# Kernel optimization log

Measured on AMD Instinct MI355X. Metric: run time of the kernel, lower is better.

Reference implementation:

```python
import jax, jax.numpy as jnp
import numpy as np

N_NODES = 2_000_000
IN_CH = 64
OUT_CH = 128
NUM_GRAPHS = 16384


def setup_inputs() -> dict:
    key = jax.random.key(0)
    k1, k2, k3, k4 = jax.random.split(key, 4)
    x = jax.random.normal(k1, (N_NODES, IN_CH), dtype=jnp.float32)
    segment_ids = jnp.sort(
        jax.random.randint(k2, (N_NODES,), 0, NUM_GRAPHS, dtype=jnp.int64)
    )
    # nn.Linear(in, out): weight [out, in], bias [out]
    bound = 1.0 / np.sqrt(IN_CH)
    weight = jax.random.uniform(k3, (OUT_CH, IN_CH), dtype=jnp.float32,
                                minval=-bound, maxval=bound)
    bias = jax.random.uniform(k4, (OUT_CH,), dtype=jnp.float32,
                              minval=-bound, maxval=bound)
    return {"x": x, "segment_ids": segment_ids, "weight": weight,
            "bias": bias, "num_graphs": NUM_GRAPHS}


def reference(x, segment_ids, weight, bias, num_graphs):
    # Per-graph mean pooling (segment mean), then linear embed.
    sums = jax.ops.segment_sum(x, segment_ids, num_segments=num_graphs)  # [G, d]
    counts = jax.ops.segment_sum(jnp.ones((x.shape[0],), x.dtype),
                                 segment_ids, num_segments=num_graphs)  # [G]
    means = sums / counts[:, None]                                       # [G, d]
    return means @ weight.T + bias                                        # [G, out]
```

## Files before the change

kernel.cpp:

```cpp
#include <hip/hip_runtime.h>
#include <hip/hip_bf16.h>


#define IN_CH 64
#define OUT_CH 128
#define WPB 8
#define BLOCK (WPB * 64)

typedef float f32x4 __attribute__((ext_vector_type(4)));

__global__ __launch_bounds__(BLOCK) void fused_pool_linear_kernel(
        const float* __restrict__ x, const int* __restrict__ ids,
        const float* __restrict__ W, const float* __restrict__ bias,
        float* __restrict__ out, int N, int G) {
    __shared__ float w_lds[IN_CH * 129];

    const int t  = threadIdx.x;
    const int wv = t >> 6;
    const int l  = t & 63;
    const int g  = blockIdx.x * WPB + wv;

    int s0 = 0, s1 = 0;
    if (g < G) {
        const int target = g + (l & 1);
        int lo = 0, hi = N;
        const int guess = (int)(((long long)target * (long long)N) / (long long)G);
        int wlo = guess - 4096; if (wlo < 0) wlo = 0;
        int whi = guess + 4096; if (whi > N) whi = N;
        const bool ok_lo = (wlo == 0) || (ids[wlo - 1] < target);
        const bool ok_hi = (whi == N) || (ids[whi] >= target);
        if (ok_lo && ok_hi) { lo = wlo; hi = whi; }
        while (lo < hi) {
            const int mid = (lo + hi) >> 1;
            if (ids[mid] < target) lo = mid + 1; else hi = mid;
        }
        s0 = __shfl(lo, 0);
        s1 = __shfl(lo, 1);
    }

    for (int i = t; i < OUT_CH * IN_CH; i += BLOCK) {
        const int o = i >> 6;
        const int c = i & 63;
        w_lds[c * 129 + o] = W[i];
    }
    __syncthreads();

    if (g >= G) return;

    const int rs = l >> 4;
    const int cq = (l & 15) << 2;

    float4 a0 = make_float4(0.f, 0.f, 0.f, 0.f);
    float4 a1 = make_float4(0.f, 0.f, 0.f, 0.f);
    int r = s0;
    for (; r + 8 <= s1; r += 8) {
        const f32x4 v0 = __builtin_nontemporal_load(
            reinterpret_cast<const f32x4*>(x + (size_t)(r + rs) * IN_CH + cq));
        const f32x4 v1 = __builtin_nontemporal_load(
            reinterpret_cast<const f32x4*>(x + (size_t)(r + 4 + rs) * IN_CH + cq));
        a0.x += v0.x; a0.y += v0.y; a0.z += v0.z; a0.w += v0.w;
        a1.x += v1.x; a1.y += v1.y; a1.z += v1.z; a1.w += v1.w;
    }
    if (r + 4 <= s1) {
        const f32x4 v = __builtin_nontemporal_load(
            reinterpret_cast<const f32x4*>(x + (size_t)(r + rs) * IN_CH + cq));
        a0.x += v.x; a0.y += v.y; a0.z += v.z; a0.w += v.w;
        r += 4;
    }
    if (r + rs < s1) {
        const f32x4 v = __builtin_nontemporal_load(
            reinterpret_cast<const f32x4*>(x + (size_t)(r + rs) * IN_CH + cq));
        a1.x += v.x; a1.y += v.y; a1.z += v.z; a1.w += v.w;
    }

    float sx = a0.x + a1.x;
    float sy = a0.y + a1.y;
    float sz = a0.z + a1.z;
    float sw = a0.w + a1.w;

    sx += __shfl_xor(sx, 16); sy += __shfl_xor(sy, 16);
    sz += __shfl_xor(sz, 16); sw += __shfl_xor(sw, 16);
    sx += __shfl_xor(sx, 32); sy += __shfl_xor(sy, 32);
    sz += __shfl_xor(sz, 32); sw += __shfl_xor(sw, 32);

    const float cnt = (float)(s1 - s0);
    const float m0 = sx / cnt;
    const float m1 = sy / cnt;
    const float m2 = sz / cnt;
    const float m3 = sw / cnt;

    float o0 = bias[l];
    float o1 = bias[l + 64];
    #pragma unroll
    for (int c = 0; c < IN_CH; ++c) {
        float m;
        switch (c & 3) {
            case 0:  m = __shfl(m0, c >> 2); break;
            case 1:  m = __shfl(m1, c >> 2); break;
            case 2:  m = __shfl(m2, c >> 2); break;
            default: m = __shfl(m3, c >> 2); break;
        }
        o0 = fmaf(w_lds[c * 129 + l],      m, o0);
        o1 = fmaf(w_lds[c * 129 + l + 64], m, o1);
    }
    out[(size_t)g * OUT_CH + l]      = o0;
    out[(size_t)g * OUT_CH + l + 64] = o1;
}

extern "C" void kernel_launch(void* const* d_in, const int* in_sizes, int n_in,
                              void* d_out, int out_size, void* d_ws, size_t ws_size,
                              hipStream_t stream) {
    const float* x    = (const float*)d_in[0];
    const int*   ids  = (const int*)d_in[1];
    const float* W    = (const float*)d_in[2];
    const float* bias = (const float*)d_in[3];
    float* out = (float*)d_out;

    const int N = in_sizes[1];
    const int G = out_size / OUT_CH;

    const int blocks = (G + WPB - 1) / WPB;
    fused_pool_linear_kernel<<<blocks, BLOCK, 0, stream>>>(
        x, ids, W, bias, out, N, G);
}
```

Baseline: 100.6 us.

## Split pooling into row-parallel atomic accumulation plus separate mean-linear kernel

Replaces the one-wave-per-graph fused kernel with a row-partitioned accumulation kernel: each wave streams a fixed 256-row chunk, reduces runs of equal segment ids and flushes partial sums and counts to a zeroed workspace with atomics. A second kernel computes the means and applies the linear layer from LDS-resident weights. This removes the per-graph binary search and the load imbalance from variable segment sizes. In exchange it adds a memset, a second launch, atomic traffic, and a sums buffer that is written and then read back. The old fused path is kept only as a fallback when the workspace is too small.

```diff
diff --git a/kernel.cpp b/kernel.cpp
--- a/kernel.cpp
+++ b/kernel.cpp
@@ -4,17 +4,128 @@
 
 #define IN_CH 64
 #define OUT_CH 128
+#define RPW 256
+#define ABLK 256
+#define BBLK 512
+#define BGRID 512
+
+typedef float f32x4 __attribute__((ext_vector_type(4)));
+
+__device__ __forceinline__ void flush_seg(float* __restrict__ sums,
+                                          int* __restrict__ counts,
+                                          int g, int l, int cq,
+                                          f32x4& acc, int& ccnt) {
+    float ax = acc.x, ay = acc.y, az = acc.z, aw = acc.w;
+    ax += __shfl_xor(ax, 16); ay += __shfl_xor(ay, 16);
+    az += __shfl_xor(az, 16); aw += __shfl_xor(aw, 16);
+    ax += __shfl_xor(ax, 32); ay += __shfl_xor(ay, 32);
+    az += __shfl_xor(az, 32); aw += __shfl_xor(aw, 32);
+    int tot = ccnt;
+    tot += __shfl_xor(tot, 16);
+    tot += __shfl_xor(tot, 32);
+    if (l < 16) {
+        float* p = sums + (size_t)g * IN_CH + cq;
+        atomicAdd(p + 0, ax);
+        atomicAdd(p + 1, ay);
+        atomicAdd(p + 2, az);
+        atomicAdd(p + 3, aw);
+    }
+    if (l == 0) atomicAdd(counts + g, tot);
+    acc.x = 0.f; acc.y = 0.f; acc.z = 0.f; acc.w = 0.f;
+    ccnt = 0;
+}
+
+__global__ __launch_bounds__(ABLK) void seg_accum_kernel(
+        const float* __restrict__ x, const int* __restrict__ ids,
+        float* __restrict__ sums, int* __restrict__ counts, int N) {
+    const int t = threadIdx.x;
+    const int w = blockIdx.x * (ABLK / 64) + (t >> 6);
+    const int l = t & 63;
+    const int row0 = w * RPW;
+    if (row0 >= N) return;
+    int row_end = row0 + RPW;
+    if (row_end > N) row_end = N;
+
+    const int rs = l >> 4;
+    const int cq = (l & 15) << 2;
+
+    f32x4 acc; acc.x = 0.f; acc.y = 0.f; acc.z = 0.f; acc.w = 0.f;
+    int ccnt = 0;
+    int cur_g = ids[row0];
+
+    for (int r = row0; r < row_end; r += 4) {
+        const int id = ids[r + rs];
+        const f32x4 v = __builtin_nontemporal_load(
+            reinterpret_cast<const f32x4*>(x + (size_t)(r + rs) * IN_CH + cq));
+        if (__all(id == cur_g)) {
+            acc.x += v.x; acc.y += v.y; acc.z += v.z; acc.w += v.w;
+            ++ccnt;
+        } else {
+            #pragma unroll
+            for (int k = 0; k < 4; ++k) {
+                const int gk = __shfl(id, k * 16);
+                if (gk != cur_g) {
+                    flush_seg(sums, counts, cur_g, l, cq, acc, ccnt);
+                    cur_g = gk;
+                }
+                if (rs == k) {
+                    acc.x += v.x; acc.y += v.y; acc.z += v.z; acc.w += v.w;
+                    ++ccnt;
+                }
+            }
+        }
+    }
+    flush_seg(sums, counts, cur_g, l, cq, acc, ccnt);
+}
+
+__global__ __launch_bounds__(BBLK) void mean_linear_kernel(
+        const float* __restrict__ sums, const int* __restrict__ counts,
+        const float* __restrict__ W, const float* __restrict__ bias,
+        float* __restrict__ out, int G) {
+    __shared__ float w_lds[IN_CH * 129];
+    const int t = threadIdx.x;
+    for (int i = t; i < OUT_CH * IN_CH; i += BBLK) {
+        const int o = i >> 6, c = i & 63;
+        w_lds[c * 129 + o] = W[i];
+    }
+    __syncthreads();
+
+    const int wv = t >> 6, l = t & 63;
+    const int cq = (l & 15) << 2;
+    const float b0 = bias[l], b1 = bias[l + 64];
+
+    for (int g = blockIdx.x * (BBLK / 64) + wv; g < G; g += BGRID * (BBLK / 64)) {
+        const float cnt = (float)counts[g];
+        const f32x4 s = *reinterpret_cast<const f32x4*>(
+            sums + (size_t)g * IN_CH + cq);
+        const float m0 = s.x / cnt, m1 = s.y / cnt;
+        const float m2 = s.z / cnt, m3 = s.w / cnt;
+
+        float o0 = b0, o1 = b1;
+        #pragma unroll
+        for (int c = 0; c < IN_CH; ++c) {
+            float m;
+            switch (c & 3) {
+                case 0:  m = __shfl(m0, c >> 2); break;
+                case 1:  m = __shfl(m1, c >> 2); break;
+                case 2:  m = __shfl(m2, c >> 2); break;
+                default: m = __shfl(m3, c >> 2); break;
+            }
+            o0 = fmaf(w_lds[c * 129 + l],      m, o0);
+            o1 = fmaf(w_lds[c * 129 + l + 64], m, o1);
+        }
+        out[(size_t)g * OUT_CH + l]      = o0;
+        out[(size_t)g * OUT_CH + l + 64] = o1;
+    }
+}
+
 #define WPB 8
 #define BLOCK (WPB * 64)
-
-typedef float f32x4 __attribute__((ext_vector_type(4)));
-
 __global__ __launch_bounds__(BLOCK) void fused_pool_linear_kernel(
         const float* __restrict__ x, const int* __restrict__ ids,
         const float* __restrict__ W, const float* __restrict__ bias,
         float* __restrict__ out, int N, int G) {
     __shared__ float w_lds[IN_CH * 129];
-
     const int t  = threadIdx.x;
     const int wv = t >> 6;
     const int l  = t & 63;
@@ -37,19 +148,15 @@
         s0 = __shfl(lo, 0);
         s1 = __shfl(lo, 1);
     }
-
     for (int i = t; i < OUT_CH * IN_CH; i += BLOCK) {
-        const int o = i >> 6;
-        const int c = i & 63;
+        const int o = i >> 6, c = i & 63;
         w_lds[c * 129 + o] = W[i];
     }
     __syncthreads();
-
     if (g >= G) return;
 
     const int rs = l >> 4;
     const int cq = (l & 15) << 2;
-
     float4 a0 = make_float4(0.f, 0.f, 0.f, 0.f);
     float4 a1 = make_float4(0.f, 0.f, 0.f, 0.f);
     int r = s0;
@@ -72,25 +179,15 @@
             reinterpret_cast<const f32x4*>(x + (size_t)(r + rs) * IN_CH + cq));
         a1.x += v.x; a1.y += v.y; a1.z += v.z; a1.w += v.w;
     }
-
-    float sx = a0.x + a1.x;
-    float sy = a0.y + a1.y;
-    float sz = a0.z + a1.z;
-    float sw = a0.w + a1.w;
-
+    float sx = a0.x + a1.x, sy = a0.y + a1.y;
+    float sz = a0.z + a1.z, sw = a0.w + a1.w;
     sx += __shfl_xor(sx, 16); sy += __shfl_xor(sy, 16);
     sz += __shfl_xor(sz, 16); sw += __shfl_xor(sw, 16);
     sx += __shfl_xor(sx, 32); sy += __shfl_xor(sy, 32);
     sz += __shfl_xor(sz, 32); sw += __shfl_xor(sw, 32);
-
     const float cnt = (float)(s1 - s0);
-    const float m0 = sx / cnt;
-    const float m1 = sy / cnt;
-    const float m2 = sz / cnt;
-    const float m3 = sw / cnt;
-
-    float o0 = bias[l];
-    float o1 = bias[l + 64];
+    const float m0 = sx / cnt, m1 = sy / cnt, m2 = sz / cnt, m3 = sw / cnt;
+    float o0 = bias[l], o1 = bias[l + 64];
     #pragma unroll
     for (int c = 0; c < IN_CH; ++c) {
         float m;
@@ -119,7 +216,20 @@
     const int N = in_sizes[1];
     const int G = out_size / OUT_CH;
 
-    const int blocks = (G + WPB - 1) / WPB;
-    fused_pool_linear_kernel<<<blocks, BLOCK, 0, stream>>>(
-        x, ids, W, bias, out, N, G);
-}
+    const size_t sums_bytes = (size_t)G * IN_CH * sizeof(float);
+    const size_t need = sums_bytes + (size_t)G * sizeof(int);
+
+    if (ws_size >= need) {
+        float* sums   = (float*)d_ws;
+        int*   counts = (int*)((char*)d_ws + sums_bytes);
+        hipMemsetAsync(d_ws, 0, need, stream);
+        const int waves   = (N + RPW - 1) / RPW;
+        const int ablocks = (waves + (ABLK / 64) - 1) / (ABLK / 64);
+        seg_accum_kernel<<<ablocks, ABLK, 0, stream>>>(x, ids, sums, counts, N);
+        mean_linear_kernel<<<BGRID, BBLK, 0, stream>>>(sums, counts, W, bias, out, G);
+    } else {
+        const int blocks = (G + WPB - 1) / WPB;
+        fused_pool_linear_kernel<<<blocks, BLOCK, 0, stream>>>(
+            x, ids, W, bias, out, N, G);
+    }
+}
```

Result: slower. 124.4 us (+23.7%).

## Split fused pool+linear into separate pooling and linear kernels via workspace

Applied to the files above, without the earlier changes.

Splits the fused kernel in two. The first pools two segments per wave, with small 256-thread blocks and no LDS, and writes the means to a workspace buffer. The second is a persistent linear kernel that loads W into LDS once per block. This removes the per-block 32KB weight staging and LDS occupancy limit from the bandwidth-bound pooling pass. The cost is an extra launch and a round-trip of the means (about 4MB) through global memory. The path only runs if the workspace is large enough; otherwise the old fused kernel is used.

```diff
diff --git a/kernel.cpp b/kernel.cpp
--- a/kernel.cpp
+++ b/kernel.cpp
@@ -4,17 +4,143 @@
 
 #define IN_CH 64
 #define OUT_CH 128
+#define GPW 2
+#define PBLK 256
+#define LBLK 512
+#define LGRID 512
+
+typedef float f32x4 __attribute__((ext_vector_type(4)));
+
+__device__ __forceinline__ void stream_seg(const float* __restrict__ x,
+                                           int s0, int s1, int rs, int cq,
+                                           float& sx, float& sy,
+                                           float& sz, float& sw) {
+    float4 a0 = make_float4(0.f, 0.f, 0.f, 0.f);
+    float4 a1 = make_float4(0.f, 0.f, 0.f, 0.f);
+    int r = s0;
+    for (; r + 8 <= s1; r += 8) {
+        const f32x4 v0 = __builtin_nontemporal_load(
+            reinterpret_cast<const f32x4*>(x + (size_t)(r + rs) * IN_CH + cq));
+        const f32x4 v1 = __builtin_nontemporal_load(
+            reinterpret_cast<const f32x4*>(x + (size_t)(r + 4 + rs) * IN_CH + cq));
+        a0.x += v0.x; a0.y += v0.y; a0.z += v0.z; a0.w += v0.w;
+        a1.x += v1.x; a1.y += v1.y; a1.z += v1.z; a1.w += v1.w;
+    }
+    if (r + 4 <= s1) {
+        const f32x4 v = __builtin_nontemporal_load(
+            reinterpret_cast<const f32x4*>(x + (size_t)(r + rs) * IN_CH + cq));
+        a0.x += v.x; a0.y += v.y; a0.z += v.z; a0.w += v.w;
+        r += 4;
+    }
+    if (r + rs < s1) {
+        const f32x4 v = __builtin_nontemporal_load(
+            reinterpret_cast<const f32x4*>(x + (size_t)(r + rs) * IN_CH + cq));
+        a1.x += v.x; a1.y += v.y; a1.z += v.z; a1.w += v.w;
+    }
+    sx = a0.x + a1.x; sy = a0.y + a1.y;
+    sz = a0.z + a1.z; sw = a0.w + a1.w;
+    sx += __shfl_xor(sx, 16); sy += __shfl_xor(sy, 16);
+    sz += __shfl_xor(sz, 16); sw += __shfl_xor(sw, 16);
+    sx += __shfl_xor(sx, 32); sy += __shfl_xor(sy, 32);
+    sz += __shfl_xor(sz, 32); sw += __shfl_xor(sw, 32);
+}
+
+__global__ __launch_bounds__(PBLK, 8) void pool_kernel(
+        const float* __restrict__ x, const int* __restrict__ ids,
+        float* __restrict__ means, int N, int G) {
+    const int t  = threadIdx.x;
+    const int w  = blockIdx.x * (PBLK / 64) + (t >> 6);
+    const int l  = t & 63;
+    const int g0 = w * GPW;
+    if (g0 >= G) return;
+
+    const int tgt = g0 + ((l < 2) ? l : 2);
+    int lo = 0, hi = N;
+    {
+        const int guess = (int)(((long long)tgt * (long long)N) / (long long)G);
+        int wlo = guess - 4096; if (wlo < 0) wlo = 0;
+        int whi = guess + 4096; if (whi > N) whi = N;
+        const bool ok_lo = (wlo == 0) || (ids[wlo - 1] < tgt);
+        const bool ok_hi = (whi == N) || (ids[whi] >= tgt);
+        if (ok_lo && ok_hi) { lo = wlo; hi = whi; }
+        while (lo < hi) {
+            const int mid = (lo + hi) >> 1;
+            if (ids[mid] < tgt) lo = mid + 1; else hi = mid;
+        }
+    }
+    const int s0 = __shfl(lo, 0);
+    const int s1 = __shfl(lo, 1);
+    const int s2 = __shfl(lo, 2);
+
+    const int rs = l >> 4;
+    const int cq = (l & 15) << 2;
+
+    float sx, sy, sz, sw;
+
+    stream_seg(x, s0, s1, rs, cq, sx, sy, sz, sw);
+    {
+        const float cnt = (float)(s1 - s0);
+        if (l < 16) {
+            f32x4 m; m.x = sx / cnt; m.y = sy / cnt; m.z = sz / cnt; m.w = sw / cnt;
+            *reinterpret_cast<f32x4*>(means + (size_t)g0 * IN_CH + cq) = m;
+        }
+    }
+
+    if (g0 + 1 < G) {
+        stream_seg(x, s1, s2, rs, cq, sx, sy, sz, sw);
+        const float cnt = (float)(s2 - s1);
+        if (l < 16) {
+            f32x4 m; m.x = sx / cnt; m.y = sy / cnt; m.z = sz / cnt; m.w = sw / cnt;
+            *reinterpret_cast<f32x4*>(means + (size_t)(g0 + 1) * IN_CH + cq) = m;
+        }
+    }
+}
+
+__global__ __launch_bounds__(LBLK) void linear_kernel(
+        const float* __restrict__ means, const float* __restrict__ W,
+        const float* __restrict__ bias, float* __restrict__ out, int G) {
+    __shared__ float w_lds[IN_CH * 129];
+    const int t = threadIdx.x;
+    for (int i = t; i < OUT_CH * IN_CH; i += LBLK) {
+        const int o = i >> 6, c = i & 63;
+        w_lds[c * 129 + o] = W[i];
+    }
+    __syncthreads();
+
+    const int wv = t >> 6, l = t & 63;
+    const int cq = (l & 15) << 2;
+    const float b0 = bias[l], b1 = bias[l + 64];
+
+    for (int g = blockIdx.x * (LBLK / 64) + wv; g < G; g += LGRID * (LBLK / 64)) {
+        const f32x4 s = *reinterpret_cast<const f32x4*>(
+            means + (size_t)g * IN_CH + cq);
+        const float m0 = s.x, m1 = s.y, m2 = s.z, m3 = s.w;
+
+        float o0 = b0, o1 = b1;
+        #pragma unroll
+        for (int c = 0; c < IN_CH; ++c) {
+            float m;
+            switch (c & 3) {
+                case 0:  m = __shfl(m0, c >> 2); break;
+                case 1:  m = __shfl(m1, c >> 2); break;
+                case 2:  m = __shfl(m2, c >> 2); break;
+                default: m = __shfl(m3, c >> 2); break;
+            }
+            o0 = fmaf(w_lds[c * 129 + l],      m, o0);
+            o1 = fmaf(w_lds[c * 129 + l + 64], m, o1);
+        }
+        out[(size_t)g * OUT_CH + l]      = o0;
+        out[(size_t)g * OUT_CH + l + 64] = o1;
+    }
+}
+
 #define WPB 8
 #define BLOCK (WPB * 64)
-
-typedef float f32x4 __attribute__((ext_vector_type(4)));
-
 __global__ __launch_bounds__(BLOCK) void fused_pool_linear_kernel(
         const float* __restrict__ x, const int* __restrict__ ids,
         const float* __restrict__ W, const float* __restrict__ bias,
         float* __restrict__ out, int N, int G) {
     __shared__ float w_lds[IN_CH * 129];
-
     const int t  = threadIdx.x;
     const int wv = t >> 6;
     const int l  = t & 63;
@@ -37,60 +163,20 @@
         s0 = __shfl(lo, 0);
         s1 = __shfl(lo, 1);
     }
-
     for (int i = t; i < OUT_CH * IN_CH; i += BLOCK) {
-        const int o = i >> 6;
-        const int c = i & 63;
+        const int o = i >> 6, c = i & 63;
         w_lds[c * 129 + o] = W[i];
     }
     __syncthreads();
-
     if (g >= G) return;
 
     const int rs = l >> 4;
     const int cq = (l & 15) << 2;
-
-    float4 a0 = make_float4(0.f, 0.f, 0.f, 0.f);
-    float4 a1 = make_float4(0.f, 0.f, 0.f, 0.f);
-    int r = s0;
-    for (; r + 8 <= s1; r += 8) {
-        const f32x4 v0 = __builtin_nontemporal_load(
-            reinterpret_cast<const f32x4*>(x + (size_t)(r + rs) * IN_CH + cq));
-        const f32x4 v1 = __builtin_nontemporal_load(
-            reinterpret_cast<const f32x4*>(x + (size_t)(r + 4 + rs) * IN_CH + cq));
-        a0.x += v0.x; a0.y += v0.y; a0.z += v0.z; a0.w += v0.w;
-        a1.x += v1.x; a1.y += v1.y; a1.z += v1.z; a1.w += v1.w;
-    }
-    if (r + 4 <= s1) {
-        const f32x4 v = __builtin_nontemporal_load(
-            reinterpret_cast<const f32x4*>(x + (size_t)(r + rs) * IN_CH + cq));
-        a0.x += v.x; a0.y += v.y; a0.z += v.z; a0.w += v.w;
-        r += 4;
-    }
-    if (r + rs < s1) {
-        const f32x4 v = __builtin_nontemporal_load(
-            reinterpret_cast<const f32x4*>(x + (size_t)(r + rs) * IN_CH + cq));
-        a1.x += v.x; a1.y += v.y; a1.z += v.z; a1.w += v.w;
-    }
-
-    float sx = a0.x + a1.x;
-    float sy = a0.y + a1.y;
-    float sz = a0.z + a1.z;
-    float sw = a0.w + a1.w;
-
-    sx += __shfl_xor(sx, 16); sy += __shfl_xor(sy, 16);
-    sz += __shfl_xor(sz, 16); sw += __shfl_xor(sw, 16);
-    sx += __shfl_xor(sx, 32); sy += __shfl_xor(sy, 32);
-    sz += __shfl_xor(sz, 32); sw += __shfl_xor(sw, 32);
-
+    float sx, sy, sz, sw;
+    stream_seg(x, s0, s1, rs, cq, sx, sy, sz, sw);
     const float cnt = (float)(s1 - s0);
-    const float m0 = sx / cnt;
-    const float m1 = sy / cnt;
-    const float m2 = sz / cnt;
-    const float m3 = sw / cnt;
-
-    float o0 = bias[l];
-    float o1 = bias[l + 64];
+    const float m0 = sx / cnt, m1 = sy / cnt, m2 = sz / cnt, m3 = sw / cnt;
+    float o0 = bias[l], o1 = bias[l + 64];
     #pragma unroll
     for (int c = 0; c < IN_CH; ++c) {
         float m;
@@ -119,7 +205,17 @@
     const int N = in_sizes[1];
     const int G = out_size / OUT_CH;
 
-    const int blocks = (G + WPB - 1) / WPB;
-    fused_pool_linear_kernel<<<blocks, BLOCK, 0, stream>>>(
-        x, ids, W, bias, out, N, G);
-}
+    const size_t means_bytes = (size_t)G * IN_CH * sizeof(float);
+
+    if (ws_size >= means_bytes) {
+        float* means = (float*)d_ws;
+        const int waves   = (G + GPW - 1) / GPW;
+        const int pblocks = (waves + (PBLK / 64) - 1) / (PBLK / 64);
+        pool_kernel<<<pblocks, PBLK, 0, stream>>>(x, ids, means, N, G);
+        linear_kernel<<<LGRID, LBLK, 0, stream>>>(means, W, bias, out, G);
+    } else {
+        const int blocks = (G + WPB - 1) / WPB;
+        fused_pool_linear_kernel<<<blocks, BLOCK, 0, stream>>>(
+            x, ids, W, bias, out, N, G);
+    }
+}
```

Measured after the change: 119.0 us. +18.3%, slower.

## Drop LDS weight staging and read weights directly from global via vector loads

Applied to the files above, without the earlier changes.

Removes the per-block transposed copy of the 128x64 weight matrix into shared memory and the block barrier. Each lane now reads its two weight rows straight from global memory with 16-byte vector loads, which should mostly hit in cache. Blocks shrink from 8 waves to 2, which cuts redundant weight staging per block. The cost is more global/L2 traffic for weights, and each lane's row-strided weight reads are uncoalesced.

```diff
diff --git a/kernel.cpp b/kernel.cpp
--- a/kernel.cpp
+++ b/kernel.cpp
@@ -4,104 +4,97 @@
 
 #define IN_CH 64
 #define OUT_CH 128
-#define WPB 8
-#define BLOCK (WPB * 64)
+#define TBLK 128
 
 typedef float f32x4 __attribute__((ext_vector_type(4)));
 
-__global__ __launch_bounds__(BLOCK) void fused_pool_linear_kernel(
+__device__ __forceinline__ f32x4 ntload(const float* p) {
+    return __builtin_nontemporal_load(reinterpret_cast<const f32x4*>(p));
+}
+
+__device__ __forceinline__ void stream_seg(const float* __restrict__ x,
+                                           int s0, int s1, int rs, int cq,
+                                           float& sx, float& sy,
+                                           float& sz, float& sw) {
+    float4 a0 = make_float4(0.f, 0.f, 0.f, 0.f);
+    float4 a1 = make_float4(0.f, 0.f, 0.f, 0.f);
+    int r = s0;
+    for (; r + 8 <= s1; r += 8) {
+        const f32x4 v0 = ntload(x + (size_t)(r + rs)     * IN_CH + cq);
+        const f32x4 v1 = ntload(x + (size_t)(r + 4 + rs) * IN_CH + cq);
+        a0.x += v0.x; a0.y += v0.y; a0.z += v0.z; a0.w += v0.w;
+        a1.x += v1.x; a1.y += v1.y; a1.z += v1.z; a1.w += v1.w;
+    }
+    if (r + 4 <= s1) {
+        const f32x4 v = ntload(x + (size_t)(r + rs) * IN_CH + cq);
+        a0.x += v.x; a0.y += v.y; a0.z += v.z; a0.w += v.w;
+        r += 4;
+    }
+    if (r + rs < s1) {
+        const f32x4 v = ntload(x + (size_t)(r + rs) * IN_CH + cq);
+        a1.x += v.x; a1.y += v.y; a1.z += v.z; a1.w += v.w;
+    }
+    sx = a0.x + a1.x; sy = a0.y + a1.y;
+    sz = a0.z + a1.z; sw = a0.w + a1.w;
+    sx += __shfl_xor(sx, 16); sy += __shfl_xor(sy, 16);
+    sz += __shfl_xor(sz, 16); sw += __shfl_xor(sw, 16);
+    sx += __shfl_xor(sx, 32); sy += __shfl_xor(sy, 32);
+    sz += __shfl_xor(sz, 32); sw += __shfl_xor(sw, 32);
+}
+
+__global__ __launch_bounds__(TBLK) void fused_nolds_kernel(
         const float* __restrict__ x, const int* __restrict__ ids,
         const float* __restrict__ W, const float* __restrict__ bias,
         float* __restrict__ out, int N, int G) {
-    __shared__ float w_lds[IN_CH * 129];
-
     const int t  = threadIdx.x;
     const int wv = t >> 6;
     const int l  = t & 63;
-    const int g  = blockIdx.x * WPB + wv;
+    const int g  = blockIdx.x * (TBLK / 64) + wv;
+    if (g >= G) return;
 
-    int s0 = 0, s1 = 0;
-    if (g < G) {
-        const int target = g + (l & 1);
-        int lo = 0, hi = N;
-        const int guess = (int)(((long long)target * (long long)N) / (long long)G);
+    const int tgt = g + (l & 1);
+    int lo = 0, hi = N;
+    {
+        const int guess = (int)(((long long)tgt * (long long)N) / (long long)G);
         int wlo = guess - 4096; if (wlo < 0) wlo = 0;
         int whi = guess + 4096; if (whi > N) whi = N;
-        const bool ok_lo = (wlo == 0) || (ids[wlo - 1] < target);
-        const bool ok_hi = (whi == N) || (ids[whi] >= target);
+        const bool ok_lo = (wlo == 0) || (ids[wlo - 1] < tgt);
+        const bool ok_hi = (whi == N) || (ids[whi] >= tgt);
         if (ok_lo && ok_hi) { lo = wlo; hi = whi; }
         while (lo < hi) {
             const int mid = (lo + hi) >> 1;
-            if (ids[mid] < target) lo = mid + 1; else hi = mid;
+            if (ids[mid] < tgt) lo = mid + 1; else hi = mid;
         }
-        s0 = __shfl(lo, 0);
-        s1 = __shfl(lo, 1);
     }
-
-    for (int i = t; i < OUT_CH * IN_CH; i += BLOCK) {
-        const int o = i >> 6;
-        const int c = i & 63;
-        w_lds[c * 129 + o] = W[i];
-    }
-    __syncthreads();
-
-    if (g >= G) return;
+    const int s0 = __shfl(lo, 0);
+    const int s1 = __shfl(lo, 1);
 
     const int rs = l >> 4;
     const int cq = (l & 15) << 2;
 
-    float4 a0 = make_float4(0.f, 0.f, 0.f, 0.f);
-    float4 a1 = make_float4(0.f, 0.f, 0.f, 0.f);
-    int r = s0;
-    for (; r + 8 <= s1; r += 8) {
-        const f32x4 v0 = __builtin_nontemporal_load(
-            reinterpret_cast<const f32x4*>(x + (size_t)(r + rs) * IN_CH + cq));
-        const f32x4 v1 = __builtin_nontemporal_load(
-            reinterpret_cast<const f32x4*>(x + (size_t)(r + 4 + rs) * IN_CH + cq));
-        a0.x += v0.x; a0.y += v0.y; a0.z += v0.z; a0.w += v0.w;
-        a1.x += v1.x; a1.y += v1.y; a1.z += v1.z; a1.w += v1.w;
-    }
-    if (r + 4 <= s1) {
-        const f32x4 v = __builtin_nontemporal_load(
-            reinterpret_cast<const f32x4*>(x + (size_t)(r + rs) * IN_CH + cq));
-        a0.x += v.x; a0.y += v.y; a0.z += v.z; a0.w += v.w;
-        r += 4;
-    }
-    if (r + rs < s1) {
-        const f32x4 v = __builtin_nontemporal_load(
-            reinterpret_cast<const f32x4*>(x + (size_t)(r + rs) * IN_CH + cq));
-        a1.x += v.x; a1.y += v.y; a1.z += v.z; a1.w += v.w;
-    }
+    float sx, sy, sz, sw;
+    stream_seg(x, s0, s1, rs, cq, sx, sy, sz, sw);
+    const float cnt = (float)(s1 - s0);
+    const float m0 = sx / cnt, m1 = sy / cnt;
+    const float m2 = sz / cnt, m3 = sw / cnt;
 
-    float sx = a0.x + a1.x;
-    float sy = a0.y + a1.y;
-    float sz = a0.z + a1.z;
-    float sw = a0.w + a1.w;
-
-    sx += __shfl_xor(sx, 16); sy += __shfl_xor(sy, 16);
-    sz += __shfl_xor(sz, 16); sw += __shfl_xor(sw, 16);
-    sx += __shfl_xor(sx, 32); sy += __shfl_xor(sy, 32);
-    sz += __shfl_xor(sz, 32); sw += __shfl_xor(sw, 32);
-
-    const float cnt = (float)(s1 - s0);
-    const float m0 = sx / cnt;
-    const float m1 = sy / cnt;
-    const float m2 = sz / cnt;
-    const float m3 = sw / cnt;
-
+    const float* w0 = W + (size_t)l        * IN_CH;
+    const float* w1 = W + (size_t)(l + 64) * IN_CH;
     float o0 = bias[l];
     float o1 = bias[l + 64];
     #pragma unroll
-    for (int c = 0; c < IN_CH; ++c) {
-        float m;
-        switch (c & 3) {
-            case 0:  m = __shfl(m0, c >> 2); break;
-            case 1:  m = __shfl(m1, c >> 2); break;
-            case 2:  m = __shfl(m2, c >> 2); break;
-            default: m = __shfl(m3, c >> 2); break;
-        }
-        o0 = fmaf(w_lds[c * 129 + l],      m, o0);
-        o1 = fmaf(w_lds[c * 129 + l + 64], m, o1);
+    for (int c4 = 0; c4 < IN_CH; c4 += 4) {
+        const f32x4 wa = *reinterpret_cast<const f32x4*>(w0 + c4);
+        const f32x4 wb = *reinterpret_cast<const f32x4*>(w1 + c4);
+        const int   src = c4 >> 2;
+        const float mm0 = __shfl(m0, src);
+        const float mm1 = __shfl(m1, src);
+        const float mm2 = __shfl(m2, src);
+        const float mm3 = __shfl(m3, src);
+        o0 = fmaf(wa.x, mm0, o0); o0 = fmaf(wa.y, mm1, o0);
+        o0 = fmaf(wa.z, mm2, o0); o0 = fmaf(wa.w, mm3, o0);
+        o1 = fmaf(wb.x, mm0, o1); o1 = fmaf(wb.y, mm1, o1);
+        o1 = fmaf(wb.z, mm2, o1); o1 = fmaf(wb.w, mm3, o1);
     }
     out[(size_t)g * OUT_CH + l]      = o0;
     out[(size_t)g * OUT_CH + l + 64] = o1;
@@ -119,7 +112,6 @@
     const int N = in_sizes[1];
     const int G = out_size / OUT_CH;
 
-    const int blocks = (G + WPB - 1) / WPB;
-    fused_pool_linear_kernel<<<blocks, BLOCK, 0, stream>>>(
-        x, ids, W, bias, out, N, G);
+    const int blocks = (G + (TBLK / 64) - 1) / (TBLK / 64);
+    fused_nolds_kernel<<<blocks, TBLK, 0, stream>>>(x, ids, W, bias, out, N, G);
 }
```

After: 163.3 us. 1.62x slower.
